# Kernel optimization log

Hardware: AMD Instinct MI355X
Metric: run time of the kernel (lower is better)

Reference implementation:

```python
import jax, jax.numpy as jnp
import numpy as np

N = 262144  # collocation points


def _glorot(k, shape):
    lim = np.sqrt(6.0 / (shape[0] + shape[1])).astype(np.float32)
    return jax.random.uniform(k, shape, jnp.float32, -lim, lim)


def setup_inputs() -> dict:
    key = jax.random.key(0)
    ks = jax.random.split(key, 5)
    # x = (z, t, theta); z in [0, 50] per bc_mask in the source
    x = jax.random.uniform(ks[0], (N, 3), jnp.float32, 0.0, 50.0)
    return {
        "x": x,
        "W1": _glorot(ks[1], (3, 128)),   "b1": jnp.zeros((128,), jnp.float32),
        "W2": _glorot(ks[2], (128, 128)), "b2": jnp.zeros((128,), jnp.float32),
        "W3": _glorot(ks[3], (128, 64)),  "b3": jnp.zeros((64,), jnp.float32),
        "W4": _glorot(ks[4], (64, 1)),    "b4": jnp.zeros((1,), jnp.float32),
    }


def _mlp(x, W1, b1, W2, b2, W3, b3, W4, b4):
    h = jnp.tanh(x @ W1 + b1)
    h = jnp.tanh(h @ W2 + b2)
    h = jnp.tanh(h @ W3 + b3)
    return (h @ W4 + b4)[..., 0]  # [N]


def reference(x, W1, b1, W2, b2, W3, b3, W4, b4):
    f = lambda xx: _mlp(xx, W1, b1, W2, b2, W3, b3, W4, b4)
    ez = jnp.broadcast_to(jnp.array([1.0, 0.0, 0.0], jnp.float32), x.shape)
    et = jnp.broadcast_to(jnp.array([0.0, 1.0, 0.0], jnp.float32), x.shape)
    # Forward + first derivatives via forward-mode JVP (per-example directional derivs)
    T, dT_dz = jax.jvp(f, (x,), (ez,))
    dT_dt = jax.jvp(f, (x,), (et,))[1]
    # Second derivative d2T/dz2: JVP of the z-directional-derivative function
    g = lambda xx: jax.jvp(f, (xx,), (jnp.broadcast_to(jnp.array([1.0, 0.0, 0.0], jnp.float32), xx.shape),))[1]
    d2T_dz2 = jax.jvp(g, (x,), (ez,))[1]
    return jnp.stack([T, dT_dz, dT_dt, d2T_dz2], axis=-1)  # [N, 4]
```

## Files before the change

### kernel.cpp

```cpp
#include <hip/hip_runtime.h>

typedef __attribute__((ext_vector_type(8))) _Float16 half8;
typedef __attribute__((ext_vector_type(4))) float f32x4;
typedef __attribute__((ext_vector_type(4))) unsigned int u32x4;
typedef unsigned short u16;
typedef unsigned int u32;

#define BLOCK 256
#define WPB 4
#define GRID 768

#define OFF_W2F 0
#define OFF_W3F 32768
#define OFF_W1  49152
#define OFF_B2  51200
#define OFF_B3  51712
#define OFF_W4  51968
#define LDS_TOTAL 52224

__device__ __forceinline__ float tanh_fast(float x) {
    float e = __expf(2.0f * x);
    return fmaf(-2.0f, __builtin_amdgcn_rcpf(e + 1.0f), 1.0f);
}
__device__ __forceinline__ u16 f2h(float f) {
    union { _Float16 h; u16 u; } t; t.h = (_Float16)f; return t.u;
}
__device__ __forceinline__ u32 pk_f16(float lo, float hi) {
    u32 a, b, r;
    asm("v_cvt_f16_f32 %0, %1" : "=v"(a) : "v"(lo));
    asm("v_cvt_f16_f32 %0, %1" : "=v"(b) : "v"(hi));
    asm("v_pack_b32_f16 %0, %1, %2" : "=v"(r) : "v"(a), "v"(b));
    return r;
}
__device__ __forceinline__ half8 as_h8(u32x4 v) {
    union { u32x4 u; half8 h; } t; t.u = v; return t.h;
}
#define MFMA16(acc, a, b) acc = __builtin_amdgcn_mfma_f32_16x16x32_f16(a, b, acc, 0, 0, 0)

__global__ __launch_bounds__(BLOCK, 3) void pinn_mfma(
    const float* __restrict__ x,
    const float* __restrict__ W1, const float* __restrict__ b1,
    const float* __restrict__ W2, const float* __restrict__ b2,
    const float* __restrict__ W3, const float* __restrict__ b3,
    const float* __restrict__ W4, const float* __restrict__ b4,
    float* __restrict__ out, int N)
{
    extern __shared__ char smem[];
    u16* w2f = (u16*)(smem + OFF_W2F);
    u16* w3f = (u16*)(smem + OFF_W3F);
    f32x4* w1v = (f32x4*)(smem + OFF_W1);
    f32x4* b2v = (f32x4*)(smem + OFF_B2);
    f32x4* b3v = (f32x4*)(smem + OFF_B3);
    f32x4* w4v = (f32x4*)(smem + OFF_W4);

    for (int s = threadIdx.x; s < 128 * 128; s += BLOCK) {
        int k = s >> 7, n = s & 127;
        int kf = k >> 5, qq = (k >> 3) & 3, j = k & 7;
        int nt = n >> 4, ee = n & 15;
        w2f[((nt * 4 + kf) * 64 + qq * 16 + ee) * 8 + j] = f2h(W2[s]);
    }
    for (int s = threadIdx.x; s < 128 * 64; s += BLOCK) {
        int fsrc = s >> 6, n = s & 63;
        int A = fsrc >> 4, qq = (fsrc >> 2) & 3, bb = fsrc & 3;
        int i = A * 4 + bb;
        int kf = i >> 3, j = i & 7;
        int nt3 = n >> 4, ee = n & 15;
        w3f[((nt3 * 4 + kf) * 64 + qq * 16 + ee) * 8 + j] = f2h(W3[s]);
    }
    for (int t = threadIdx.x; t < 128; t += BLOCK)
        w1v[t] = (f32x4){W1[t], W1[128 + t], W1[256 + t], b1[t]};
    for (int t = threadIdx.x; t < 32; t += BLOCK) {
        int f = (t >> 2) * 16 + (t & 3) * 4;
        b2v[t] = (f32x4){b2[f], b2[f + 1], b2[f + 2], b2[f + 3]};
    }
    for (int t = threadIdx.x; t < 16; t += BLOCK) {
        int f = (t >> 2) * 16 + (t & 3) * 4;
        b3v[t] = (f32x4){b3[f], b3[f + 1], b3[f + 2], b3[f + 3]};
        w4v[t] = (f32x4){W4[f], W4[f + 1], W4[f + 2], W4[f + 3]};
    }
    __syncthreads();

    const int lane = threadIdx.x & 63;
    const int wv = threadIdx.x >> 6;
    const int q = lane >> 4;
    const int e = lane & 15;
    const float b4v = b4[0];

    const u16* w2l = w2f + lane * 8;
    const u16* w3l = w3f + lane * 8;

    const int ntiles = N >> 4;
    const int gw = blockIdx.x * WPB + wv;
    const int nw = gridDim.x * WPB;

    for (int tile = gw; tile < ntiles; tile += nw) {
        const int gbase = tile << 4;

        half8 Hv[4], Ha[4], Ht[4], Hc[4];
        {
            const float* xp = x + 3 * (size_t)(gbase + e);
            float x0 = xp[0], x1 = xp[1], x2 = xp[2];
#pragma unroll
            for (int kf = 0; kf < 4; kf++) {
                u32 pv[4], pa[4], pt[4], pc[4];
#pragma unroll
                for (int jp = 0; jp < 4; jp++) {
                    f32x4 wA = w1v[kf * 32 + q * 8 + 2 * jp];
                    f32x4 wB = w1v[kf * 32 + q * 8 + 2 * jp + 1];
                    float z0 = fmaf(x0, wA[0], fmaf(x1, wA[1], fmaf(x2, wA[2], wA[3])));
                    float z1 = fmaf(x0, wB[0], fmaf(x1, wB[1], fmaf(x2, wB[2], wB[3])));
                    float h0 = tanh_fast(z0), h1 = tanh_fast(z1);
                    float g0 = fmaf(-h0, h0, 1.0f), g1 = fmaf(-h1, h1, 1.0f);
                    pv[jp] = pk_f16(h0, h1);
                    pa[jp] = pk_f16(g0 * wA[0], g1 * wB[0]);
                    pt[jp] = pk_f16(g0 * wA[1], g1 * wB[1]);
                    float c0 = -2.0f * h0 * g0 * wA[0] * wA[0];
                    float c1 = -2.0f * h1 * g1 * wB[0] * wB[0];
                    pc[jp] = pk_f16(c0, c1);
                }
                Hv[kf] = as_h8((u32x4){pv[0], pv[1], pv[2], pv[3]});
                Ha[kf] = as_h8((u32x4){pa[0], pa[1], pa[2], pa[3]});
                Ht[kf] = as_h8((u32x4){pt[0], pt[1], pt[2], pt[3]});
                Hc[kf] = as_h8((u32x4){pc[0], pc[1], pc[2], pc[3]});
            }
        }

        u32x4 A3v[4], A3a[4], A3t[4], A3c[4];
#pragma unroll
        for (int nt = 0; nt < 8; nt++) {
            f32x4 acv = b2v[nt * 4 + q];
            f32x4 aca = {0.f, 0.f, 0.f, 0.f};
            f32x4 act = {0.f, 0.f, 0.f, 0.f};
            f32x4 acc_ = {0.f, 0.f, 0.f, 0.f};
#pragma unroll
            for (int kf = 0; kf < 4; kf++) {
                half8 Wk = *(const half8*)(w2l + (nt * 4 + kf) * 512);
                MFMA16(acv, Wk, Hv[kf]);
                MFMA16(aca, Wk, Ha[kf]);
                MFMA16(act, Wk, Ht[kf]);
                MFMA16(acc_, Wk, Hc[kf]);
            }
            float hh[4], na[4], ntv[4], nc[4];
#pragma unroll
            for (int r = 0; r < 4; r++) {
                float h = tanh_fast(acv[r]);
                float g = fmaf(-h, h, 1.0f);
                hh[r] = h;
                na[r] = g * aca[r];
                ntv[r] = g * act[r];
                nc[r] = fmaf(-2.0f * h * g * aca[r], aca[r], g * acc_[r]);
            }
            const int kf3 = nt >> 1, s0 = (nt & 1) * 2;
            A3v[kf3][s0]     = pk_f16(hh[0], hh[1]);
            A3v[kf3][s0 + 1] = pk_f16(hh[2], hh[3]);
            A3a[kf3][s0]     = pk_f16(na[0], na[1]);
            A3a[kf3][s0 + 1] = pk_f16(na[2], na[3]);
            A3t[kf3][s0]     = pk_f16(ntv[0], ntv[1]);
            A3t[kf3][s0 + 1] = pk_f16(ntv[2], ntv[3]);
            A3c[kf3][s0]     = pk_f16(nc[0], nc[1]);
            A3c[kf3][s0 + 1] = pk_f16(nc[2], nc[3]);
        }

        float sT = 0.f, sA = 0.f, sTt = 0.f, sC = 0.f;
#pragma unroll
        for (int nt3 = 0; nt3 < 4; nt3++) {
            f32x4 v3 = b3v[nt3 * 4 + q];
            f32x4 a3 = {0.f, 0.f, 0.f, 0.f};
            f32x4 t3 = {0.f, 0.f, 0.f, 0.f};
            f32x4 c3 = {0.f, 0.f, 0.f, 0.f};
#pragma unroll
            for (int kf = 0; kf < 4; kf++) {
                half8 Wk = *(const half8*)(w3l + (nt3 * 4 + kf) * 512);
                MFMA16(v3, Wk, as_h8(A3v[kf]));
                MFMA16(a3, Wk, as_h8(A3a[kf]));
                MFMA16(t3, Wk, as_h8(A3t[kf]));
                MFMA16(c3, Wk, as_h8(A3c[kf]));
            }
            f32x4 w4q = w4v[nt3 * 4 + q];
#pragma unroll
            for (int r = 0; r < 4; r++) {
                float h = tanh_fast(v3[r]);
                float g = fmaf(-h, h, 1.0f);
                sT  = fmaf(h, w4q[r], sT);
                sA  = fmaf(g * a3[r], w4q[r], sA);
                sTt = fmaf(g * t3[r], w4q[r], sTt);
                float cc = fmaf(-2.0f * h * g * a3[r], a3[r], g * c3[r]);
                sC  = fmaf(cc, w4q[r], sC);
            }
        }

        sT  += __shfl_xor(sT, 16);  sT  += __shfl_xor(sT, 32);
        sA  += __shfl_xor(sA, 16);  sA  += __shfl_xor(sA, 32);
        sTt += __shfl_xor(sTt, 16); sTt += __shfl_xor(sTt, 32);
        sC  += __shfl_xor(sC, 16);  sC  += __shfl_xor(sC, 32);
        if (lane < 16) {
            *(float4*)(out + 4 * (size_t)(gbase + e)) =
                make_float4(sT + b4v, sA, sTt, sC);
        }
    }
}

extern "C" void kernel_launch(void* const* d_in, const int* in_sizes, int n_in,
                              void* d_out, int out_size, void* d_ws, size_t ws_size,
                              hipStream_t stream) {
    const float* x  = (const float*)d_in[0];
    const float* W1 = (const float*)d_in[1];
    const float* b1 = (const float*)d_in[2];
    const float* W2 = (const float*)d_in[3];
    const float* b2 = (const float*)d_in[4];
    const float* W3 = (const float*)d_in[5];
    const float* b3 = (const float*)d_in[6];
    const float* W4 = (const float*)d_in[7];
    const float* b4 = (const float*)d_in[8];
    float* out = (float*)d_out;
    int N = in_sizes[0] / 3;

    (void)hipFuncSetAttribute((const void*)pinn_mfma,
                              hipFuncAttributeMaxDynamicSharedMemorySize, LDS_TOTAL);
    hipLaunchKernelGGL(pinn_mfma, dim3(GRID), dim3(BLOCK), LDS_TOTAL, stream,
                       x, W1, b1, W2, b2, W3, b3, W4, b4, out, N);
}
```

Measured before the change: 141.3 us.

## Use atomic work-stealing tile scheduler and XOR-swizzle W1 LDS layout

Replaces the static grid-stride tile assignment with a global atomic counter, so each wavefront fetches its next 16-row tile dynamically, prefetching the next index one iteration ahead. This is meant to balance load across waves and CUs at the tail. It also XOR-swizzles the W1/b1 LDS layout by quad index to reduce LDS bank conflicts on the per-lane f32x4 reads. The cost is one atomic per tile per wave plus an extra memset launch to reset the counter, which the timer may include.

```diff
diff --git a/kernel.cpp b/kernel.cpp
--- a/kernel.cpp
+++ b/kernel.cpp
@@ -37,18 +37,23 @@
 }
 #define MFMA16(acc, a, b) acc = __builtin_amdgcn_mfma_f32_16x16x32_f16(a, b, acc, 0, 0, 0)
 
+__device__ __forceinline__ u32 next_tile(u32* cnt, int lane) {
+    u32 t = 0;
+    if (lane == 0) t = atomicAdd(cnt, 1u);
+    return (u32)__builtin_amdgcn_readfirstlane((int)t);
+}
+
 __global__ __launch_bounds__(BLOCK, 3) void pinn_mfma(
     const float* __restrict__ x,
     const float* __restrict__ W1, const float* __restrict__ b1,
     const float* __restrict__ W2, const float* __restrict__ b2,
     const float* __restrict__ W3, const float* __restrict__ b3,
     const float* __restrict__ W4, const float* __restrict__ b4,
-    float* __restrict__ out, int N)
+    float* __restrict__ out, u32* __restrict__ cnt, int N)
 {
     extern __shared__ char smem[];
     u16* w2f = (u16*)(smem + OFF_W2F);
     u16* w3f = (u16*)(smem + OFF_W3F);
-    f32x4* w1v = (f32x4*)(smem + OFF_W1);
     f32x4* b2v = (f32x4*)(smem + OFF_B2);
     f32x4* b3v = (f32x4*)(smem + OFF_B3);
     f32x4* w4v = (f32x4*)(smem + OFF_W4);
@@ -67,8 +72,10 @@
         int nt3 = n >> 4, ee = n & 15;
         w3f[((nt3 * 4 + kf) * 64 + qq * 16 + ee) * 8 + j] = f2h(W3[s]);
     }
-    for (int t = threadIdx.x; t < 128; t += BLOCK)
-        w1v[t] = (f32x4){W1[t], W1[128 + t], W1[256 + t], b1[t]};
+    for (int t = threadIdx.x; t < 128; t += BLOCK) {
+        f32x4 v = (f32x4){W1[t], W1[128 + t], W1[256 + t], b1[t]};
+        *(f32x4*)(smem + OFF_W1 + ((t * 16) ^ (((t >> 3) & 3) << 5))) = v;
+    }
     for (int t = threadIdx.x; t < 32; t += BLOCK) {
         int f = (t >> 2) * 16 + (t & 3) * 4;
         b2v[t] = (f32x4){b2[f], b2[f + 1], b2[f + 2], b2[f + 3]};
@@ -81,20 +88,20 @@
     __syncthreads();
 
     const int lane = threadIdx.x & 63;
-    const int wv = threadIdx.x >> 6;
     const int q = lane >> 4;
     const int e = lane & 15;
+    const int qx = q << 5;
     const float b4v = b4[0];
 
     const u16* w2l = w2f + lane * 8;
     const u16* w3l = w3f + lane * 8;
 
-    const int ntiles = N >> 4;
-    const int gw = blockIdx.x * WPB + wv;
-    const int nw = gridDim.x * WPB;
-
-    for (int tile = gw; tile < ntiles; tile += nw) {
-        const int gbase = tile << 4;
+    const u32 ntiles = (u32)(N >> 4);
+
+    u32 tile = next_tile(cnt, lane);
+    while (tile < ntiles) {
+        const u32 nxt = next_tile(cnt, lane);
+        const int gbase = (int)(tile << 4);
 
         half8 Hv[4], Ha[4], Ht[4], Hc[4];
         {
@@ -105,8 +112,9 @@
                 u32 pv[4], pa[4], pt[4], pc[4];
 #pragma unroll
                 for (int jp = 0; jp < 4; jp++) {
-                    f32x4 wA = w1v[kf * 32 + q * 8 + 2 * jp];
-                    f32x4 wB = w1v[kf * 32 + q * 8 + 2 * jp + 1];
+                    int idx = kf * 32 + q * 8 + 2 * jp;
+                    f32x4 wA = *(const f32x4*)(smem + OFF_W1 + ((idx * 16) ^ qx));
+                    f32x4 wB = *(const f32x4*)(smem + OFF_W1 + (((idx + 1) * 16) ^ qx));
                     float z0 = fmaf(x0, wA[0], fmaf(x1, wA[1], fmaf(x2, wA[2], wA[3])));
                     float z1 = fmaf(x0, wB[0], fmaf(x1, wB[1], fmaf(x2, wB[2], wB[3])));
                     float h0 = tanh_fast(z0), h1 = tanh_fast(z1);
@@ -197,6 +205,8 @@
             *(float4*)(out + 4 * (size_t)(gbase + e)) =
                 make_float4(sT + b4v, sA, sTt, sC);
         }
+
+        tile = nxt;
     }
 }
 
@@ -213,10 +223,12 @@
     const float* W4 = (const float*)d_in[7];
     const float* b4 = (const float*)d_in[8];
     float* out = (float*)d_out;
+    u32* cnt = (u32*)d_ws;
     int N = in_sizes[0] / 3;
 
+    (void)hipMemsetAsync(cnt, 0, sizeof(u32), stream);
     (void)hipFuncSetAttribute((const void*)pinn_mfma,
                               hipFuncAttributeMaxDynamicSharedMemorySize, LDS_TOTAL);
     hipLaunchKernelGGL(pinn_mfma, dim3(GRID), dim3(BLOCK), LDS_TOTAL, stream,
-                       x, W1, b1, W2, b2, W3, b3, W4, b4, out, N);
-}
+                       x, W1, b1, W2, b2, W3, b3, W4, b4, out, cnt, N);
+}
```

Measured after the change: 317.4 us. +124.7%, slower.
